# Kernel tuning notes

Hardware: AMD Instinct MI355X
Metric: run time of the kernel (lower is better)

## Reference

```python
import jax, jax.numpy as jnp
import numpy as np

D = 1024  # repr_dims


def setup_inputs() -> dict:
    key = jax.random.key(0)
    ks = jax.random.split(key, 10)
    B, T = 32, 2048
    inp = {
        "raw_residual": jax.random.normal(ks[0], (B, T, D), jnp.float32),
        "rel_residual": jax.random.normal(ks[1], (B, T, D), jnp.float32),
        "raw_global": jax.random.normal(ks[2], (B, D), jnp.float32),
        "spec_global": jax.random.normal(ks[3], (B, D), jnp.float32),
        "relation_global": jax.random.normal(ks[4], (B, D), jnp.float32),
        # LayerNorm(3D) params
        "ln_gamma": jnp.ones((3 * D,), jnp.float32),
        "ln_beta": jnp.zeros((3 * D,), jnp.float32),
        # Linear(3D -> D)
        "w1": jax.random.normal(ks[5], (3 * D, D), jnp.float32) * (1.0 / np.sqrt(3 * D)),
        "b1": jnp.zeros((D,), jnp.float32),
        # Linear(D -> 1), bias init -2.1972246 per module
        "w2": jax.random.normal(ks[6], (D, 1), jnp.float32) * (1.0 / np.sqrt(D)),
        "b2": jnp.full((1,), -2.1972246, jnp.float32),
    }
    return inp


def reference(raw_residual, rel_residual, raw_global, spec_global, relation_global,
              ln_gamma, ln_beta, w1, b1, w2, b2):
    # Concatenate globals: [B, 3D]
    g = jnp.concatenate([raw_global, spec_global, relation_global], axis=-1)
    # LayerNorm (eps=1e-5, like torch default)
    mu = jnp.mean(g, axis=-1, keepdims=True)
    var = jnp.mean(jnp.square(g - mu), axis=-1, keepdims=True)
    g = (g - mu) * jax.lax.rsqrt(var + 1e-5) * ln_gamma + ln_beta
    # 2-layer MLP gate with exact (erf) GELU, then sigmoid -> alpha [B, 1]
    h = jax.nn.gelu(g @ w1 + b1, approximate=False)
    alpha = jax.nn.sigmoid(h @ w2 + b2)
    # Scaled residual add: alpha broadcast over the sequence axis (dim 1)
    main_repr = raw_residual + alpha[:, None, :] * rel_residual
    return main_repr, alpha
```

## Files before the change

kernel.cpp:

```cpp
#include <hip/hip_runtime.h>
#include <hip/hip_bf16.h>
#include <math.h>

#define D_ 1024
#define THREE_D 3072
#define B_ 32
#define T_ 2048

__global__ __launch_bounds__(256) void ln_kernel(
    const float* __restrict__ raw_g, const float* __restrict__ spec_g,
    const float* __restrict__ rel_g, const float* __restrict__ gamma,
    const float* __restrict__ beta, float* __restrict__ gnT) {
  const int b = blockIdx.x;
  const int tid = threadIdx.x;
  __shared__ float sg[THREE_D];
  __shared__ float red[8];
  __shared__ float stats[2];

  float s = 0.f, s2 = 0.f;
#pragma unroll
  for (int i = 0; i < 12; ++i) {
    int k = i * 256 + tid;
    float v;
    if (k < 1024)       v = raw_g[b * 1024 + k];
    else if (k < 2048)  v = spec_g[b * 1024 + (k - 1024)];
    else                v = rel_g[b * 1024 + (k - 2048)];
    sg[k] = v;
    s += v;
    s2 += v * v;
  }
#pragma unroll
  for (int off = 32; off; off >>= 1) {
    s  += __shfl_down(s, off, 64);
    s2 += __shfl_down(s2, off, 64);
  }
  const int wv = tid >> 6;
  if ((tid & 63) == 0) { red[wv] = s; red[4 + wv] = s2; }
  __syncthreads();
  if (tid == 0) {
    float ts  = red[0] + red[1] + red[2] + red[3];
    float ts2 = red[4] + red[5] + red[6] + red[7];
    float mu  = ts * (1.0f / THREE_D);
    float var = ts2 * (1.0f / THREE_D) - mu * mu;
    stats[0] = mu;
    stats[1] = rsqrtf(var + 1e-5f);
  }
  __syncthreads();
  const float mu = stats[0], rstd = stats[1];
#pragma unroll
  for (int i = 0; i < 12; ++i) {
    int k = i * 256 + tid;
    gnT[k * 32 + b] = (sg[k] - mu) * rstd * gamma[k] + beta[k];
  }
}

__global__ __launch_bounds__(256) void gate_gemm(
    const float* __restrict__ gnT, const float* __restrict__ w1,
    float* __restrict__ partials) {
  const int lane = threadIdx.x & 63;
  const int wvid = threadIdx.x >> 6;
  const int j = blockIdx.x * 64 + lane;
  const int slice = blockIdx.y * 4 + wvid;
  const int k0 = slice * 48;

  float4 acc[8];
#pragma unroll
  for (int i = 0; i < 8; ++i) acc[i] = make_float4(0.f, 0.f, 0.f, 0.f);

  for (int kk = 0; kk < 48; ++kk) {
    const int k = k0 + kk;
    const float wv = w1[k * D_ + j];
    const float4* gp = (const float4*)(gnT + k * 32);
#pragma unroll
    for (int i = 0; i < 8; ++i) {
      float4 g = gp[i];
      acc[i].x = fmaf(g.x, wv, acc[i].x);
      acc[i].y = fmaf(g.y, wv, acc[i].y);
      acc[i].z = fmaf(g.z, wv, acc[i].z);
      acc[i].w = fmaf(g.w, wv, acc[i].w);
    }
  }
  float* base = partials + (size_t)slice * (B_ * D_) + j;
#pragma unroll
  for (int i = 0; i < 8; ++i) {
    base[(4 * i + 0) * D_] = acc[i].x;
    base[(4 * i + 1) * D_] = acc[i].y;
    base[(4 * i + 2) * D_] = acc[i].z;
    base[(4 * i + 3) * D_] = acc[i].w;
  }
}

__global__ __launch_bounds__(256) void gate_finish(
    const float* __restrict__ partials, const float* __restrict__ b1,
    const float* __restrict__ w2, const float* __restrict__ b2,
    float* __restrict__ alpha_out) {
  const int b = blockIdx.x;
  const int tid = threadIdx.x;
  float contrib = 0.f;
#pragma unroll
  for (int i = 0; i < 4; ++i) {
    const int j = i * 256 + tid;
    float s = b1[j];
    for (int sl = 0; sl < 64; ++sl)
      s += partials[((size_t)sl * B_ + b) * D_ + j];
    float h = 0.5f * s * (1.0f + erff(s * 0.7071067811865476f));
    contrib += h * w2[j];
  }
  __shared__ float red[4];
#pragma unroll
  for (int off = 32; off; off >>= 1) contrib += __shfl_down(contrib, off, 64);
  if ((tid & 63) == 0) red[tid >> 6] = contrib;
  __syncthreads();
  if (tid == 0) {
    float tot = red[0] + red[1] + red[2] + red[3] + b2[0];
    alpha_out[b] = 1.0f / (1.0f + expf(-tot));
  }
}

__global__ __launch_bounds__(256) void fuse_kernel(
    const float4* __restrict__ raw, const float4* __restrict__ rel,
    const float* __restrict__ alpha, float4* __restrict__ out) {
  const int b = blockIdx.y;
  const float a = alpha[b];
  const size_t f4_per_b = (size_t)T_ * D_ / 4;
  size_t i0 = (size_t)b * f4_per_b + (size_t)blockIdx.x * 256 + threadIdx.x;
  size_t i1 = i0 + f4_per_b / 2;
  float4 r0 = raw[i0], e0 = rel[i0];
  float4 r1 = raw[i1], e1 = rel[i1];
  float4 o0, o1;
  o0.x = fmaf(a, e0.x, r0.x); o0.y = fmaf(a, e0.y, r0.y);
  o0.z = fmaf(a, e0.z, r0.z); o0.w = fmaf(a, e0.w, r0.w);
  o1.x = fmaf(a, e1.x, r1.x); o1.y = fmaf(a, e1.y, r1.y);
  o1.z = fmaf(a, e1.z, r1.z); o1.w = fmaf(a, e1.w, r1.w);
  out[i0] = o0;
  out[i1] = o1;
}

extern "C" void kernel_launch(void* const* d_in, const int* in_sizes, int n_in,
                              void* d_out, int out_size, void* d_ws, size_t ws_size,
                              hipStream_t stream) {
  const float* raw_res = (const float*)d_in[0];
  const float* rel_res = (const float*)d_in[1];
  const float* raw_g   = (const float*)d_in[2];
  const float* spec_g  = (const float*)d_in[3];
  const float* rel_g   = (const float*)d_in[4];
  const float* gamma   = (const float*)d_in[5];
  const float* beta    = (const float*)d_in[6];
  const float* w1      = (const float*)d_in[7];
  const float* b1      = (const float*)d_in[8];
  const float* w2      = (const float*)d_in[9];
  const float* b2      = (const float*)d_in[10];

  float* out = (float*)d_out;
  float* gnT      = out;
  float* partials = out + 131072;
  float* alpha    = out + (size_t)B_ * T_ * D_;

  ln_kernel<<<dim3(B_), dim3(256), 0, stream>>>(raw_g, spec_g, rel_g, gamma, beta, gnT);
  gate_gemm<<<dim3(16, 16), dim3(256), 0, stream>>>(gnT, w1, partials);
  gate_finish<<<dim3(B_), dim3(256), 0, stream>>>(partials, b1, w2, b2, alpha);
  fuse_kernel<<<dim3(1024, B_), dim3(256), 0, stream>>>(
      (const float4*)raw_res, (const float4*)rel_res, alpha, (float4*)d_out);
}
```

Baseline: 636.3 us.

## Restructure gate GEMM with LDS staging and widen streaming fuse kernel

The gate GEMM now stages the normalized globals in shared memory, preloads 48 w1 values per thread into registers, and splits the batch across wave pairs. The gate finish kernel is spread over more blocks per batch row and combines its results with an atomicAdd into a pre-alpha buffer, followed by a tiny sigmoid kernel. The dominant fuse kernel processes four float4 per thread and uses nontemporal stores to avoid cache pollution. Most of the time sits in the bandwidth-bound fuse pass, so the main lever is the store hint, at the cost of one extra launch and atomic ordering nondeterminism.

```diff
diff --git a/kernel.cpp b/kernel.cpp
--- a/kernel.cpp
+++ b/kernel.cpp
@@ -1,5 +1,4 @@
 #include <hip/hip_runtime.h>
-#include <hip/hip_bf16.h>
 #include <math.h>
 
 #define D_ 1024
@@ -7,15 +6,20 @@
 #define B_ 32
 #define T_ 2048
 
+typedef float floatx4 __attribute__((ext_vector_type(4)));
+
 __global__ __launch_bounds__(256) void ln_kernel(
     const float* __restrict__ raw_g, const float* __restrict__ spec_g,
     const float* __restrict__ rel_g, const float* __restrict__ gamma,
-    const float* __restrict__ beta, float* __restrict__ gnT) {
+    const float* __restrict__ beta, float* __restrict__ gnT,
+    float* __restrict__ pre_alpha) {
   const int b = blockIdx.x;
   const int tid = threadIdx.x;
   __shared__ float sg[THREE_D];
   __shared__ float red[8];
   __shared__ float stats[2];
+
+  if (tid == 0) pre_alpha[b] = 0.f;
 
   float s = 0.f, s2 = 0.f;
 #pragma unroll
@@ -54,35 +58,52 @@
   }
 }
 
-__global__ __launch_bounds__(256) void gate_gemm(
+__global__ __launch_bounds__(512) void gate_gemm(
     const float* __restrict__ gnT, const float* __restrict__ w1,
     float* __restrict__ partials) {
-  const int lane = threadIdx.x & 63;
-  const int wvid = threadIdx.x >> 6;
-  const int j = blockIdx.x * 64 + lane;
-  const int slice = blockIdx.y * 4 + wvid;
-  const int k0 = slice * 48;
-
-  float4 acc[8];
-#pragma unroll
-  for (int i = 0; i < 8; ++i) acc[i] = make_float4(0.f, 0.f, 0.f, 0.f);
-
+  const int tid   = threadIdx.x;
+  const int lane  = tid & 63;
+  const int wvid  = tid >> 6;
+  const int khalf = wvid >> 1;
+  const int bhalf = wvid & 1;
+  const int jt = blockIdx.x;
+  const int by = blockIdx.y;
+  const int j  = jt * 64 + lane;
+  const int kslice = by * 4 + khalf;
+
+  __shared__ float sg[192 * 32];
+  const float* gsrc = gnT + by * 192 * 32;
+#pragma unroll
+  for (int i = 0; i < 12; ++i) sg[i * 512 + tid] = gsrc[i * 512 + tid];
+  __syncthreads();
+
+  const float* wrow = w1 + (size_t)kslice * 48 * D_ + j;
+  float w[48];
+#pragma unroll
+  for (int kk = 0; kk < 48; ++kk) w[kk] = wrow[(size_t)kk * D_];
+
+  float4 acc[4];
+#pragma unroll
+  for (int i = 0; i < 4; ++i) acc[i] = make_float4(0.f, 0.f, 0.f, 0.f);
+
+  const float4* gp = (const float4*)(sg + (khalf * 48) * 32 + bhalf * 16);
+#pragma unroll
   for (int kk = 0; kk < 48; ++kk) {
-    const int k = k0 + kk;
-    const float wv = w1[k * D_ + j];
-    const float4* gp = (const float4*)(gnT + k * 32);
-#pragma unroll
-    for (int i = 0; i < 8; ++i) {
-      float4 g = gp[i];
-      acc[i].x = fmaf(g.x, wv, acc[i].x);
-      acc[i].y = fmaf(g.y, wv, acc[i].y);
-      acc[i].z = fmaf(g.z, wv, acc[i].z);
-      acc[i].w = fmaf(g.w, wv, acc[i].w);
+    const float4* g = gp + kk * 8;
+    const float wv_ = w[kk];
+#pragma unroll
+    for (int i = 0; i < 4; ++i) {
+      float4 gv = g[i];
+      acc[i].x = fmaf(gv.x, wv_, acc[i].x);
+      acc[i].y = fmaf(gv.y, wv_, acc[i].y);
+      acc[i].z = fmaf(gv.z, wv_, acc[i].z);
+      acc[i].w = fmaf(gv.w, wv_, acc[i].w);
     }
   }
-  float* base = partials + (size_t)slice * (B_ * D_) + j;
-#pragma unroll
-  for (int i = 0; i < 8; ++i) {
+
+  float* base = partials + ((size_t)(kslice * 2 + bhalf) * 16) * D_ + j;
+#pragma unroll
+  for (int i = 0; i < 4; ++i) {
     base[(4 * i + 0) * D_] = acc[i].x;
     base[(4 * i + 1) * D_] = acc[i].y;
     base[(4 * i + 2) * D_] = acc[i].z;
@@ -92,48 +113,68 @@
 
 __global__ __launch_bounds__(256) void gate_finish(
     const float* __restrict__ partials, const float* __restrict__ b1,
-    const float* __restrict__ w2, const float* __restrict__ b2,
+    const float* __restrict__ w2, float* __restrict__ pre_alpha) {
+  const int jc  = blockIdx.x;
+  const int b   = blockIdx.y;
+  const int tid = threadIdx.x;
+  const int j   = jc * 256 + tid;
+  const int bh  = b >> 4, br = b & 15;
+
+  const float* p = partials + ((size_t)bh * 16 + br) * D_ + j;
+  float s = b1[j];
+#pragma unroll 8
+  for (int sl = 0; sl < 64; ++sl)
+    s += p[(size_t)sl * 32768];
+  float h = 0.5f * s * (1.0f + erff(s * 0.7071067811865476f));
+  float c = h * w2[j];
+
+#pragma unroll
+  for (int off = 32; off; off >>= 1) c += __shfl_down(c, off, 64);
+  __shared__ float red[4];
+  if ((tid & 63) == 0) red[tid >> 6] = c;
+  __syncthreads();
+  if (tid == 0)
+    atomicAdd(&pre_alpha[b], red[0] + red[1] + red[2] + red[3]);
+}
+
+__global__ __launch_bounds__(64) void alphify(
+    const float* __restrict__ pre_alpha, const float* __restrict__ b2,
     float* __restrict__ alpha_out) {
-  const int b = blockIdx.x;
   const int tid = threadIdx.x;
-  float contrib = 0.f;
-#pragma unroll
-  for (int i = 0; i < 4; ++i) {
-    const int j = i * 256 + tid;
-    float s = b1[j];
-    for (int sl = 0; sl < 64; ++sl)
-      s += partials[((size_t)sl * B_ + b) * D_ + j];
-    float h = 0.5f * s * (1.0f + erff(s * 0.7071067811865476f));
-    contrib += h * w2[j];
-  }
-  __shared__ float red[4];
-#pragma unroll
-  for (int off = 32; off; off >>= 1) contrib += __shfl_down(contrib, off, 64);
-  if ((tid & 63) == 0) red[tid >> 6] = contrib;
-  __syncthreads();
-  if (tid == 0) {
-    float tot = red[0] + red[1] + red[2] + red[3] + b2[0];
-    alpha_out[b] = 1.0f / (1.0f + expf(-tot));
+  if (tid < B_) {
+    float t = pre_alpha[tid] + b2[0];
+    alpha_out[tid] = 1.0f / (1.0f + expf(-t));
   }
 }
 
 __global__ __launch_bounds__(256) void fuse_kernel(
     const float4* __restrict__ raw, const float4* __restrict__ rel,
-    const float* __restrict__ alpha, float4* __restrict__ out) {
+    const float* __restrict__ alpha, float* __restrict__ out) {
   const int b = blockIdx.y;
   const float a = alpha[b];
   const size_t f4_per_b = (size_t)T_ * D_ / 4;
-  size_t i0 = (size_t)b * f4_per_b + (size_t)blockIdx.x * 256 + threadIdx.x;
-  size_t i1 = i0 + f4_per_b / 2;
-  float4 r0 = raw[i0], e0 = rel[i0];
-  float4 r1 = raw[i1], e1 = rel[i1];
-  float4 o0, o1;
+  const size_t base = (size_t)b * f4_per_b + (size_t)blockIdx.x * 1024 + threadIdx.x;
+
+  float4 r0 = raw[base +   0], r1 = raw[base + 256],
+         r2 = raw[base + 512], r3 = raw[base + 768];
+  float4 e0 = rel[base +   0], e1 = rel[base + 256],
+         e2 = rel[base + 512], e3 = rel[base + 768];
+
+  floatx4 o0, o1, o2, o3;
   o0.x = fmaf(a, e0.x, r0.x); o0.y = fmaf(a, e0.y, r0.y);
   o0.z = fmaf(a, e0.z, r0.z); o0.w = fmaf(a, e0.w, r0.w);
   o1.x = fmaf(a, e1.x, r1.x); o1.y = fmaf(a, e1.y, r1.y);
   o1.z = fmaf(a, e1.z, r1.z); o1.w = fmaf(a, e1.w, r1.w);
-  out[i0] = o0;
-  out[i1] = o1;
+  o2.x = fmaf(a, e2.x, r2.x); o2.y = fmaf(a, e2.y, r2.y);
+  o2.z = fmaf(a, e2.z, r2.z); o2.w = fmaf(a, e2.w, r2.w);
+  o3.x = fmaf(a, e3.x, r3.x); o3.y = fmaf(a, e3.y, r3.y);
+  o3.z = fmaf(a, e3.z, r3.z); o3.w = fmaf(a, e3.w, r3.w);
+
+  floatx4* o = reinterpret_cast<floatx4*>(out) + base;
+  __builtin_nontemporal_store(o0, o +   0);
+  __builtin_nontemporal_store(o1, o + 256);
+  __builtin_nontemporal_store(o2, o + 512);
+  __builtin_nontemporal_store(o3, o + 768);
 }
 
 extern "C" void kernel_launch(void* const* d_in, const int* in_sizes, int n_in,
@@ -152,13 +193,16 @@
   const float* b2      = (const float*)d_in[10];
 
   float* out = (float*)d_out;
-  float* gnT      = out;
-  float* partials = out + 131072;
-  float* alpha    = out + (size_t)B_ * T_ * D_;
-
-  ln_kernel<<<dim3(B_), dim3(256), 0, stream>>>(raw_g, spec_g, rel_g, gamma, beta, gnT);
-  gate_gemm<<<dim3(16, 16), dim3(256), 0, stream>>>(gnT, w1, partials);
-  gate_finish<<<dim3(B_), dim3(256), 0, stream>>>(partials, b1, w2, b2, alpha);
-  fuse_kernel<<<dim3(1024, B_), dim3(256), 0, stream>>>(
-      (const float4*)raw_res, (const float4*)rel_res, alpha, (float4*)d_out);
-}
+  float* gnT       = out;
+  float* pre_alpha = out + 120000;
+  float* partials  = out + 131072;
+  float* alpha     = out + (size_t)B_ * T_ * D_;
+
+  ln_kernel<<<dim3(B_), dim3(256), 0, stream>>>(raw_g, spec_g, rel_g, gamma, beta,
+                                                gnT, pre_alpha);
+  gate_gemm<<<dim3(16, 16), dim3(512), 0, stream>>>(gnT, w1, partials);
+  gate_finish<<<dim3(4, B_), dim3(256), 0, stream>>>(partials, b1, w2, pre_alpha);
+  alphify<<<dim3(1), dim3(64), 0, stream>>>(pre_alpha, b2, alpha);
+  fuse_kernel<<<dim3(512, B_), dim3(256), 0, stream>>>(
+      (const float4*)raw_res, (const float4*)rel_res, alpha, d_out ? (float*)d_out : nullptr);
+}
```

Result: no change. 626.8 us (-1.5%).
